# Kernel optimization log

Hardware: AMD Instinct MI355X
Metric: run time of the kernel (lower is better)

Reference implementation:

```python
import jax, jax.numpy as jnp
import numpy as np
from jax import lax

EPS = 1e-5  # torch BatchNorm2d default eps


def _binconv(x, w, b):
    # BinarizeConv2d: sign-binarize input and weight, dense conv, then add bias
    y = lax.conv_general_dilated(jnp.sign(x), jnp.sign(w), (2, 2), [(1, 1), (1, 1)],
                                 dimension_numbers=('NCHW', 'OIHW', 'NCHW'))
    return y + b[None, :, None, None]


def _bn(x, g, be):
    # BatchNorm2d in training mode: biased batch statistics over (N,H,W)
    m = jnp.mean(x, axis=(0, 2, 3), keepdims=True)
    v = jnp.mean((x - m) ** 2, axis=(0, 2, 3), keepdims=True)
    return (x - m) * (g[None, :, None, None] / jnp.sqrt(v + EPS)) + be[None, :, None, None]


def setup_inputs() -> dict:
    key = jax.random.key(0)
    ks = jax.random.split(key, 20)
    B = 8192
    d = {"x": jax.random.normal(ks[0], (B, 6, 32, 48), jnp.float32)}
    chans = [(12, 6), (24, 12), (48, 24), (96, 48)]
    i = 1
    for n, (co, ci) in enumerate(chans, 1):
        d[f"w{n}"] = jax.random.normal(ks[i], (co, ci, 5, 5), jnp.float32) * 0.1; i += 1
        d[f"b{n}"] = jax.random.normal(ks[i], (co,), jnp.float32) * 0.01; i += 1
        d[f"g{n}"] = jnp.ones((co,), jnp.float32)
        d[f"be{n}"] = jnp.zeros((co,), jnp.float32)
    d["wl"] = jax.random.normal(ks[i], (360, 192), jnp.float32) * 0.1; i += 1
    d["bl"] = jax.random.normal(ks[i], (360,), jnp.float32) * 0.01
    return d


def reference(x, w1, b1, g1, be1, w2, b2, g2, be2, w3, b3, g3, be3,
              w4, b4, g4, be4, wl, bl):
    x1 = jnp.clip(_bn(_binconv(x, w1, b1), g1, be1), 0.0, 1.0)
    x2 = jnp.clip(_bn(_binconv(x1, w2, b2), g2, be2), 0.0, 1.0)
    x3 = jnp.clip(_bn(_binconv(x2, w3, b3), g3, be3), 0.0, 1.0)
    x4 = jnp.clip(_bn(_binconv(x3, w4, b4), g4, be4), 0.0, 1.0)
    x4 = x4.reshape(-1, 192)  # (B, 96*1*2)
    # BinarizeLinear: in_features=192 != 784 so input is binarized too
    return jnp.sign(x4) @ jnp.sign(wl).T + bl
```

## Files before the change

### kernel.cpp

```cpp
#include <hip/hip_runtime.h>
#include <stdint.h>

typedef unsigned long long u64;
typedef uint32_t u32;
typedef uint16_t u16;

#define NIMG 8192

static const size_t O_TOT = 0;
static const size_t O_X1  = 4096;
static const size_t O_A2  = O_X1 + (size_t)NIMG*32*50*2;
static const size_t O_A3  = O_A2 + (size_t)NIMG*15*25*2;
static const size_t O_A4  = O_A3 + (size_t)NIMG*7*13*4;
static const size_t O_AL  = O_A4 + (size_t)NIMG*3*7*8;
static const size_t O_W1  = O_AL + (size_t)NIMG*3*8;
static const size_t O_W2  = O_W1 + 120*8;
static const size_t O_W3  = O_W2 + 240*8;
static const size_t O_W4  = O_W3 + 960*8;
static const size_t O_WL  = O_W4 + 3840*8;
static const size_t O_S   = O_WL + 2160*8;

__global__ void pack_w_k(const float* w1, const float* w2, const float* w3,
                         const float* w4, const float* wl,
                         u64* W1, u64* W2, u64* W3, u64* W4, u64* WL, u64* tot) {
  if (blockIdx.x == 5) {
    int t = threadIdx.x;
    tot[t] = 0; tot[t+256] = 0;
    return;
  }
  int u = blockIdx.x*256 + threadIdx.x;
  if (u < 60) {
    int co = u/5, kh = u%5;
    u64 wp=0, wn=0;
    for (int kw=0; kw<5; kw++) for (int ci=0; ci<6; ci++) {
      float v = w1[co*150 + ci*25 + kh*5 + kw];
      int pos = 6*kw + ci;
      if (v > 0.f) wp |= 1ull<<pos; else if (v < 0.f) wn |= 1ull<<pos;
    }
    W1[u*2]   = wp | (wn<<32);
    W1[u*2+1] = wn | (wp<<32);
  } else if (u < 180) {
    int t = u-60; int co=t/5, kh=t%5;
    u64 wp=0, wn=0;
    for (int kw=0; kw<5; kw++) for (int ci=0; ci<12; ci++) {
      float v = w2[co*300 + ci*25 + kh*5 + kw];
      int pos = 12*kw+ci;
      if (v>0.f) wp |= 1ull<<pos; else if (v<0.f) wn |= 1ull<<pos;
    }
    W2[t*2] = wp; W2[t*2+1] = wn;
  } else if (u < 420) {
    int t = u-180; int co=t/5, kh=t%5;
    u64 wp[2]={0,0}, wn[2]={0,0};
    for (int kw=0; kw<5; kw++) for (int ci=0; ci<24; ci++) {
      float v = w3[co*600 + ci*25 + kh*5 + kw];
      int pos = 24*kw+ci;
      if (v>0.f) wp[pos>>6] |= 1ull<<(pos&63); else if (v<0.f) wn[pos>>6] |= 1ull<<(pos&63);
    }
    W3[t*4]=wp[0]; W3[t*4+1]=wp[1]; W3[t*4+2]=wn[0]; W3[t*4+3]=wn[1];
  } else if (u < 900) {
    int t = u-420; int co=t/5, kh=t%5;
    u64 wp[4]={0,0,0,0}, wn[4]={0,0,0,0};
    for (int kw=0; kw<5; kw++) for (int ci=0; ci<48; ci++) {
      float v = w4[co*1200 + ci*25 + kh*5 + kw];
      int pos = 48*kw+ci;
      if (v>0.f) wp[pos>>6] |= 1ull<<(pos&63); else if (v<0.f) wn[pos>>6] |= 1ull<<(pos&63);
    }
    for (int j=0;j<4;j++){ W4[t*8+j]=wp[j]; W4[t*8+4+j]=wn[j]; }
  } else if (u < 1260) {
    int o = u-900;
    u64 wp[3]={0,0,0}, wn[3]={0,0,0};
    for (int k=0;k<192;k++){
      float v = wl[o*192+k];
      if (v>0.f) wp[k>>6] |= 1ull<<(k&63); else if (v<0.f) wn[k>>6] |= 1ull<<(k&63);
    }
    for (int j=0;j<3;j++){ WL[o*6+j]=wp[j]; WL[o*6+3+j]=wn[j]; }
  }
}

__global__ __launch_bounds__(256) void binx_k(const float* __restrict__ x, u16* __restrict__ X1) {
  int gid = blockIdx.x*256+threadIdx.x;
  int n = gid / 1536, r = gid % 1536, h = r/48, w = r%48;
  const float* xp = x + (size_t)n*9216 + h*48 + w;
  u32 v = 0;
  #pragma unroll
  for (int c=0;c<6;c++){ float t = xp[c*1536];
    v |= (t>0.f ? 1u:0u)<<c; v |= (t<0.f ? 1u:0u)<<(8+c); }
  u16* row = X1 + (size_t)n*1600 + h*50;
  row[w+1] = (u16)v;
  if (w==0)  row[0]  = 0;
  if (w==47) row[49] = 0;
}

__global__ __launch_bounds__(256) void conv1_k(const u16* __restrict__ X1, const u64* __restrict__ W1,
                                               u32* __restrict__ S1) {
  int pix = blockIdx.x*256+threadIdx.x;
  int n = pix/345, r = pix%345, oh = r/23, ow = r%23;
  int S[12];
  #pragma unroll
  for (int i=0;i<12;i++) S[i]=0;
  const u16* base = X1 + (size_t)n*1600;
  for (int kh=0; kh<5; kh++){
    int row = 2*oh-1+kh;
    if ((unsigned)row >= 32u) continue;
    const u16* p = base + row*50 + 2*ow;
    u64 xp=0, xn=0;
    #pragma unroll
    for (int i=0;i<5;i++){ u32 v = p[i];
      xp |= (u64)(v & 63u) << (6*i);
      xn |= (u64)(v >> 8)  << (6*i); }
    u64 X = xp | (xn<<32);
    const u64* wr = W1 + kh*2;
    #pragma unroll
    for (int co=0;co<12;co++)
      S[co] += __popcll(X & wr[co*10]) - __popcll(X & wr[co*10+1]);
  }
  u32* o = S1 + (size_t)pix*3;
  #pragma unroll
  for (int j=0;j<3;j++)
    o[j] = (u32)(S[4*j]&255) | ((u32)(S[4*j+1]&255)<<8) |
           ((u32)(S[4*j+2]&255)<<16) | ((u32)(S[4*j+3]&255)<<24);
}

__global__ __launch_bounds__(256) void conv2_k(const u16* __restrict__ A2, const u64* __restrict__ W2,
                                               short* __restrict__ S2) {
  int pix = blockIdx.x*256+threadIdx.x;
  int n = pix/77, r = pix%77, oh = r/11, ow = r%11;
  int S[24];
  #pragma unroll
  for (int i=0;i<24;i++) S[i]=0;
  const u16* base = A2 + (size_t)n*375;
  for (int kh=0; kh<5; kh++){
    int row = 2*oh-1+kh;
    if ((unsigned)row >= 15u) continue;
    const u16* p = base + row*25 + 2*ow;
    u64 X=0;
    #pragma unroll
    for (int i=0;i<5;i++) X |= (u64)p[i] << (12*i);
    const u64* wr = W2 + kh*2;
    #pragma unroll
    for (int co=0;co<24;co++)
      S[co] += __popcll(X & wr[co*10]) - __popcll(X & wr[co*10+1]);
  }
  short* o = S2 + (size_t)pix*24;
  #pragma unroll
  for (int co=0;co<24;co++) o[co] = (short)S[co];
}

__global__ __launch_bounds__(256) void conv3_k(const u32* __restrict__ A3, const u64* __restrict__ W3,
                                               short* __restrict__ S3) {
  int pix = blockIdx.x*256+threadIdx.x;
  int n = pix/15, r = pix%15, oh = r/5, ow = r%5;
  int S[48];
  #pragma unroll
  for (int i=0;i<48;i++) S[i]=0;
  const u32* base = A3 + (size_t)n*91;
  for (int kh=0; kh<5; kh++){
    int row = 2*oh-1+kh;
    if ((unsigned)row >= 7u) continue;
    const u32* p = base + row*13 + 2*ow;
    u64 a0=p[0],a1=p[1],a2=p[2],a3=p[3],a4=p[4];
    u64 x0 = a0 | (a1<<24) | (a2<<48);
    u64 x1 = (a2>>16) | (a3<<8) | (a4<<32);
    const u64* wr = W3 + kh*4;
    #pragma unroll
    for (int co=0;co<48;co++){
      const u64* q = wr + co*20;
      S[co] += __popcll(x0 & q[0]) + __popcll(x1 & q[1])
             - __popcll(x0 & q[2]) - __popcll(x1 & q[3]);
    }
  }
  short* o = S3 + (size_t)pix*48;
  #pragma unroll
  for (int co=0;co<48;co++) o[co] = (short)S[co];
}

__global__ __launch_bounds__(256) void conv4_k(const u64* __restrict__ A4, const u64* __restrict__ W4,
                                               short* __restrict__ S4) {
  int gid = blockIdx.x*256+threadIdx.x;
  int pix = gid>>2, grp = gid&3;
  int n = pix>>1, ow = pix&1;
  int S[24];
  #pragma unroll
  for (int i=0;i<24;i++) S[i]=0;
  const u64* base = A4 + (size_t)n*21;
  for (int kh=0; kh<5; kh++){
    int row = kh-1;
    if ((unsigned)row >= 3u) continue;
    const u64* p = base + row*7 + 2*ow;
    u64 a0=p[0],a1=p[1],a2=p[2],a3=p[3],a4=p[4];
    u64 x0 = a0 | (a1<<48);
    u64 x1 = (a1>>16) | (a2<<32);
    u64 x2 = (a2>>32) | (a3<<16);
    u64 x3 = a4;
    const u64* wr = W4 + kh*8;
    #pragma unroll
    for (int j=0;j<24;j++){
      const u64* q = wr + (grp*24+j)*40;
      S[j] += __popcll(x0&q[0]) + __popcll(x1&q[1]) + __popcll(x2&q[2]) + __popcll(x3&q[3])
            - __popcll(x0&q[4]) - __popcll(x1&q[5]) - __popcll(x2&q[6]) - __popcll(x3&q[7]);
    }
  }
  short* o = S4 + (size_t)pix*96 + grp*24;
  #pragma unroll
  for (int j=0;j<24;j++) o[j] = (short)S[j];
}

#define LSTR 265
template<int NR>
__device__ long long tree_reduce(const int (&vals)[NR], int* lds){
  int t = threadIdx.x;
  #pragma unroll
  for (int r=0;r<NR;r++) lds[r*LSTR + t] = vals[r];
  __syncthreads();
  if (t < NR*8) {
    int r = t % NR, seg = t / NR;
    const int* row = lds + r*LSTR + seg*32;
    int s = 0;
    #pragma unroll
    for (int i=0;i<32;i++) s += row[i];
    lds[r*LSTR + 256 + seg] = s;
  }
  __syncthreads();
  long long res = 0;
  if (t < NR) {
    const int* row = lds + t*LSTR + 256;
    int s = 0;
    #pragma unroll
    for (int i=0;i<8;i++) s += row[i];
    res = s;
  }
  __syncthreads();
  return res;
}

__global__ __launch_bounds__(256) void stats1_k(const u32* __restrict__ S1, u64* __restrict__ tot){
  __shared__ int lds[24*LSTR];
  int acc[12], q[12];
  #pragma unroll
  for (int i=0;i<12;i++){ acc[i]=0; q[i]=0; }
  int nt = gridDim.x*256;
  for (int p = blockIdx.x*256+threadIdx.x; p < NIMG*345; p += nt){
    u32 w0=S1[(size_t)p*3], w1=S1[(size_t)p*3+1], w2=S1[(size_t)p*3+2];
    #pragma unroll
    for (int c=0;c<12;c++){
      u32 w = (c<4)?w0:(c<8)?w1:w2;
      int v = (int)(w << ((3-(c&3))*8)) >> 24;
      acc[c]+=v; q[c]+=v*v;
    }
  }
  int vals[24];
  #pragma unroll
  for (int c=0;c<12;c++){ vals[c]=acc[c]; vals[12+c]=q[c]; }
  long long rs = tree_reduce<24>(vals, lds);
  int t = threadIdx.x;
  if (t < 12)       atomicAdd(&tot[t*2],        (u64)rs);
  else if (t < 24)  atomicAdd(&tot[(t-12)*2+1], (u64)rs);
}

__global__ __launch_bounds__(256) void stats2_k(const short* __restrict__ S, u64* __restrict__ tot){
  __shared__ int lds[24*LSTR];
  int acc[24], q[24];
  #pragma unroll
  for (int i=0;i<24;i++){ acc[i]=0; q[i]=0; }
  int nt = gridDim.x*256;
  for (int p = blockIdx.x*256+threadIdx.x; p < NIMG*77; p += nt){
    const int4* s4 = (const int4*)(S + (size_t)p*24);
    int4 A=s4[0], B=s4[1], Cc=s4[2];
    int w[12]={A.x,A.y,A.z,A.w,B.x,B.y,B.z,B.w,Cc.x,Cc.y,Cc.z,Cc.w};
    #pragma unroll
    for (int j=0;j<12;j++){
      int v0=(int)(short)(w[j]&0xffff), v1=w[j]>>16;
      acc[2*j]+=v0; q[2*j]+=v0*v0; acc[2*j+1]+=v1; q[2*j+1]+=v1*v1;
    }
  }
  long long rs = tree_reduce<24>(acc, lds);
  int t = threadIdx.x;
  if (t < 24) atomicAdd(&tot[t*2], (u64)rs);
  rs = tree_reduce<24>(q, lds);
  if (t < 24) atomicAdd(&tot[t*2+1], (u64)rs);
}

__global__ __launch_bounds__(256) void statsP_k(const short* __restrict__ S, u64* __restrict__ tot, int C){
  __shared__ int lds[24*LSTR];
  int pix = blockIdx.x*256+threadIdx.x;
  const short* s = S + (size_t)pix*C;
  int t = threadIdx.x;
  for (int c0=0; c0<C; c0+=24){
    const int4* s4 = (const int4*)(s + c0);
    int4 A=s4[0], B=s4[1], Cc=s4[2];
    int w[12]={A.x,A.y,A.z,A.w,B.x,B.y,B.z,B.w,Cc.x,Cc.y,Cc.z,Cc.w};
    int v[24];
    #pragma unroll
    for (int j=0;j<12;j++){ v[2*j]=(int)(short)(w[j]&0xffff); v[2*j+1]=w[j]>>16; }
    long long rs = tree_reduce<24>(v, lds);
    if (t < 24) atomicAdd(&tot[(c0+t)*2], (u64)rs);
    int vq[24];
    #pragma unroll
    for (int r=0;r<24;r++) vq[r]=v[r]*v[r];
    rs = tree_reduce<24>(vq, lds);
    if (t < 24) atomicAdd(&tot[(c0+t)*2+1], (u64)rs);
  }
}

template<int C>
__device__ void bn_params(const u64* tot, const float* g, const float* be, double cnt,
                          float* s_mu, float* s_k, float* s_be) {
  int t = threadIdx.x;
  if (t < C) {
    long long sum = (long long)tot[t*2];
    long long sq  = (long long)tot[t*2+1];
    double mu  = (double)sum / cnt;
    double var = (double)sq / cnt - mu*mu;
    double kk  = (double)g[t] / sqrt(var + 1e-5);
    s_mu[t] = (float)mu; s_k[t] = (float)kk; s_be[t] = be[t];
  }
  __syncthreads();
}

__global__ __launch_bounds__(256) void thresh1_k(const u32* __restrict__ S1, const u64* tot,
                                                 const float* g, const float* be, u16* __restrict__ A2){
  __shared__ float mu[12], kk[12], bb[12];
  bn_params<12>(tot, g, be, 2826240.0, mu, kk, bb);
  int pix = blockIdx.x*256+threadIdx.x;
  int n=pix/345, r=pix%345, oh=r/23, ow=r%23;
  const u32* s = S1 + (size_t)pix*3;
  u32 w0=s[0], w1=s[1], w2=s[2];
  u32 wv=0;
  #pragma unroll
  for (int c=0;c<12;c++){
    u32 w = (c<4) ? w0 : (c<8) ? w1 : w2;
    int sv = (int)(w << ((3-(c&3))*8)) >> 24;
    float v = ((float)sv-mu[c])*kk[c]+bb[c];
    wv |= (v>0.f?1u:0u)<<c;
  }
  u16* row = A2 + (size_t)n*375 + oh*25;
  row[ow+1] = (u16)wv;
  if (ow==0)  row[0]  = 0;
  if (ow==22) row[24] = 0;
}

__global__ __launch_bounds__(256) void thresh2_k(const short* __restrict__ S2, const u64* tot,
                                                 const float* g, const float* be, u32* __restrict__ A3){
  __shared__ float mu[24], kk[24], bb[24];
  bn_params<24>(tot, g, be, 630784.0, mu, kk, bb);
  int pix = blockIdx.x*256+threadIdx.x;
  int n=pix/77, r=pix%77, oh=r/11, ow=r%11;
  const short* s = S2 + (size_t)pix*24;
  u32 wv=0;
  #pragma unroll
  for (int c=0;c<24;c++){ float v = ((float)s[c]-mu[c])*kk[c]+bb[c]; wv |= (v>0.f?1u:0u)<<c; }
  u32* row = A3 + (size_t)n*91 + oh*13;
  row[ow+1] = wv;
  if (ow==0)  row[0]  = 0;
  if (ow==10) row[12] = 0;
}

__global__ __launch_bounds__(256) void thresh3_k(const short* __restrict__ S3, const u64* tot,
                                                 const float* g, const float* be, u64* __restrict__ A4){
  __shared__ float mu[48], kk[48], bb[48];
  bn_params<48>(tot, g, be, 122880.0, mu, kk, bb);
  int pix = blockIdx.x*256+threadIdx.x;
  int n=pix/15, r=pix%15, oh=r/5, ow=r%5;
  const short* s = S3 + (size_t)pix*48;
  u64 wv=0;
  #pragma unroll
  for (int c=0;c<48;c++){ float v = ((float)s[c]-mu[c])*kk[c]+bb[c]; wv |= (u64)(v>0.f?1u:0u)<<c; }
  u64* row = A4 + (size_t)n*21 + oh*7;
  row[ow+1] = wv;
  if (ow==0) row[0] = 0;
  if (ow==4) row[6] = 0;
}

__global__ __launch_bounds__(256) void thresh4_k(const short* __restrict__ S4, const u64* tot,
                                                 const float* g, const float* be, u64* __restrict__ aL){
  __shared__ float mu[96], kk[96], bb[96];
  bn_params<96>(tot, g, be, 16384.0, mu, kk, bb);
  int n = blockIdx.x*256+threadIdx.x;
  if (n >= NIMG) return;
  u64 a[3]={0,0,0};
  for (int w=0;w<2;w++){
    const short* s = S4 + ((size_t)n*2+w)*96;
    #pragma unroll
    for (int c=0;c<96;c++){
      float v = ((float)s[c]-mu[c])*kk[c]+bb[c];
      int k = c*2+w;
      if (v>0.f) a[k>>6] |= 1ull<<(k&63);
    }
  }
  aL[(size_t)n*3]=a[0]; aL[(size_t)n*3+1]=a[1]; aL[(size_t)n*3+2]=a[2];
}

__global__ __launch_bounds__(256) void linear_k(const u64* __restrict__ aL, const u64* __restrict__ WL,
                                                const float* __restrict__ bl, float* __restrict__ out){
  int gid = blockIdx.x*256+threadIdx.x;
  int o = gid%360, n = gid/360;
  const u64* a = aL + (size_t)n*3;
  const u64* w = WL + (size_t)o*6;
  int S = __popcll(a[0]&w[0]) + __popcll(a[1]&w[1]) + __popcll(a[2]&w[2])
        - __popcll(a[0]&w[3]) - __popcll(a[1]&w[4]) - __popcll(a[2]&w[5]);
  out[gid] = (float)S + bl[o];
}

extern "C" void kernel_launch(void* const* d_in, const int* in_sizes, int n_in,
                              void* d_out, int out_size, void* d_ws, size_t ws_size,
                              hipStream_t stream) {
  const float* x  = (const float*)d_in[0];
  const float* w1 = (const float*)d_in[1];
  const float* g1 = (const float*)d_in[3];
  const float* be1= (const float*)d_in[4];
  const float* w2 = (const float*)d_in[5];
  const float* g2 = (const float*)d_in[7];
  const float* be2= (const float*)d_in[8];
  const float* w3 = (const float*)d_in[9];
  const float* g3 = (const float*)d_in[11];
  const float* be3= (const float*)d_in[12];
  const float* w4 = (const float*)d_in[13];
  const float* g4 = (const float*)d_in[15];
  const float* be4= (const float*)d_in[16];
  const float* wl = (const float*)d_in[17];
  const float* bl = (const float*)d_in[18];

  char* ws = (char*)d_ws;
  u64* tot = (u64*)(ws + O_TOT);
  u16* X1  = (u16*)(ws + O_X1);
  u16* A2  = (u16*)(ws + O_A2);
  u32* A3  = (u32*)(ws + O_A3);
  u64* A4  = (u64*)(ws + O_A4);
  u64* aL  = (u64*)(ws + O_AL);
  u64* W1  = (u64*)(ws + O_W1);
  u64* W2  = (u64*)(ws + O_W2);
  u64* W3  = (u64*)(ws + O_W3);
  u64* W4  = (u64*)(ws + O_W4);
  u64* WL  = (u64*)(ws + O_WL);
  u32*   S1b = (u32*)(ws + O_S);
  short* Sb  = (short*)(ws + O_S);

  pack_w_k<<<6,256,0,stream>>>(w1,w2,w3,w4,wl, W1,W2,W3,W4,WL, tot);
  binx_k<<<49152,256,0,stream>>>(x, X1);

  conv1_k<<<11040,256,0,stream>>>(X1, W1, S1b);
  stats1_k<<<1024,256,0,stream>>>(S1b, tot+0);
  thresh1_k<<<11040,256,0,stream>>>(S1b, tot+0, g1, be1, A2);

  conv2_k<<<2464,256,0,stream>>>(A2, W2, Sb);
  stats2_k<<<512,256,0,stream>>>(Sb, tot+24);
  thresh2_k<<<2464,256,0,stream>>>(Sb, tot+24, g2, be2, A3);

  conv3_k<<<480,256,0,stream>>>(A3, W3, Sb);
  statsP_k<<<480,256,0,stream>>>(Sb, tot+72, 48);
  thresh3_k<<<480,256,0,stream>>>(Sb, tot+72, g3, be3, A4);

  conv4_k<<<256,256,0,stream>>>(A4, W4, Sb);
  statsP_k<<<64,256,0,stream>>>(Sb, tot+168, 96);
  thresh4_k<<<32,256,0,stream>>>(Sb, tot+168, g4, be4, aL);

  linear_k<<<11520,256,0,stream>>>(aL, WL, bl, (float*)d_out);
}
```

Baseline: 869.2 us.

## Fuse binarize, conv, BN stats and threshold into per-layer kernels

```diff
diff --git a/kernel.cpp b/kernel.cpp
--- a/kernel.cpp
+++ b/kernel.cpp
@@ -8,17 +8,13 @@
 #define NIMG 8192
 
 static const size_t O_TOT = 0;
-static const size_t O_X1  = 4096;
-static const size_t O_A2  = O_X1 + (size_t)NIMG*32*50*2;
-static const size_t O_A3  = O_A2 + (size_t)NIMG*15*25*2;
-static const size_t O_A4  = O_A3 + (size_t)NIMG*7*13*4;
-static const size_t O_AL  = O_A4 + (size_t)NIMG*3*7*8;
-static const size_t O_W1  = O_AL + (size_t)NIMG*3*8;
+static const size_t O_W1  = 4096;
 static const size_t O_W2  = O_W1 + 120*8;
 static const size_t O_W3  = O_W2 + 240*8;
 static const size_t O_W4  = O_W3 + 960*8;
 static const size_t O_WL  = O_W4 + 3840*8;
-static const size_t O_S   = O_WL + 2160*8;
+static const size_t O_SA  = 65536;
+static const size_t O_SB  = O_SA + (size_t)NIMG*345*12;
 
 __global__ void pack_w_k(const float* w1, const float* w2, const float* w3,
                          const float* w4, const float* wl,
@@ -77,234 +73,9 @@
   }
 }
 
-__global__ __launch_bounds__(256) void binx_k(const float* __restrict__ x, u16* __restrict__ X1) {
-  int gid = blockIdx.x*256+threadIdx.x;
-  int n = gid / 1536, r = gid % 1536, h = r/48, w = r%48;
-  const float* xp = x + (size_t)n*9216 + h*48 + w;
-  u32 v = 0;
-  #pragma unroll
-  for (int c=0;c<6;c++){ float t = xp[c*1536];
-    v |= (t>0.f ? 1u:0u)<<c; v |= (t<0.f ? 1u:0u)<<(8+c); }
-  u16* row = X1 + (size_t)n*1600 + h*50;
-  row[w+1] = (u16)v;
-  if (w==0)  row[0]  = 0;
-  if (w==47) row[49] = 0;
-}
-
-__global__ __launch_bounds__(256) void conv1_k(const u16* __restrict__ X1, const u64* __restrict__ W1,
-                                               u32* __restrict__ S1) {
-  int pix = blockIdx.x*256+threadIdx.x;
-  int n = pix/345, r = pix%345, oh = r/23, ow = r%23;
-  int S[12];
-  #pragma unroll
-  for (int i=0;i<12;i++) S[i]=0;
-  const u16* base = X1 + (size_t)n*1600;
-  for (int kh=0; kh<5; kh++){
-    int row = 2*oh-1+kh;
-    if ((unsigned)row >= 32u) continue;
-    const u16* p = base + row*50 + 2*ow;
-    u64 xp=0, xn=0;
-    #pragma unroll
-    for (int i=0;i<5;i++){ u32 v = p[i];
-      xp |= (u64)(v & 63u) << (6*i);
-      xn |= (u64)(v >> 8)  << (6*i); }
-    u64 X = xp | (xn<<32);
-    const u64* wr = W1 + kh*2;
-    #pragma unroll
-    for (int co=0;co<12;co++)
-      S[co] += __popcll(X & wr[co*10]) - __popcll(X & wr[co*10+1]);
-  }
-  u32* o = S1 + (size_t)pix*3;
-  #pragma unroll
-  for (int j=0;j<3;j++)
-    o[j] = (u32)(S[4*j]&255) | ((u32)(S[4*j+1]&255)<<8) |
-           ((u32)(S[4*j+2]&255)<<16) | ((u32)(S[4*j+3]&255)<<24);
-}
-
-__global__ __launch_bounds__(256) void conv2_k(const u16* __restrict__ A2, const u64* __restrict__ W2,
-                                               short* __restrict__ S2) {
-  int pix = blockIdx.x*256+threadIdx.x;
-  int n = pix/77, r = pix%77, oh = r/11, ow = r%11;
-  int S[24];
-  #pragma unroll
-  for (int i=0;i<24;i++) S[i]=0;
-  const u16* base = A2 + (size_t)n*375;
-  for (int kh=0; kh<5; kh++){
-    int row = 2*oh-1+kh;
-    if ((unsigned)row >= 15u) continue;
-    const u16* p = base + row*25 + 2*ow;
-    u64 X=0;
-    #pragma unroll
-    for (int i=0;i<5;i++) X |= (u64)p[i] << (12*i);
-    const u64* wr = W2 + kh*2;
-    #pragma unroll
-    for (int co=0;co<24;co++)
-      S[co] += __popcll(X & wr[co*10]) - __popcll(X & wr[co*10+1]);
-  }
-  short* o = S2 + (size_t)pix*24;
-  #pragma unroll
-  for (int co=0;co<24;co++) o[co] = (short)S[co];
-}
-
-__global__ __launch_bounds__(256) void conv3_k(const u32* __restrict__ A3, const u64* __restrict__ W3,
-                                               short* __restrict__ S3) {
-  int pix = blockIdx.x*256+threadIdx.x;
-  int n = pix/15, r = pix%15, oh = r/5, ow = r%5;
-  int S[48];
-  #pragma unroll
-  for (int i=0;i<48;i++) S[i]=0;
-  const u32* base = A3 + (size_t)n*91;
-  for (int kh=0; kh<5; kh++){
-    int row = 2*oh-1+kh;
-    if ((unsigned)row >= 7u) continue;
-    const u32* p = base + row*13 + 2*ow;
-    u64 a0=p[0],a1=p[1],a2=p[2],a3=p[3],a4=p[4];
-    u64 x0 = a0 | (a1<<24) | (a2<<48);
-    u64 x1 = (a2>>16) | (a3<<8) | (a4<<32);
-    const u64* wr = W3 + kh*4;
-    #pragma unroll
-    for (int co=0;co<48;co++){
-      const u64* q = wr + co*20;
-      S[co] += __popcll(x0 & q[0]) + __popcll(x1 & q[1])
-             - __popcll(x0 & q[2]) - __popcll(x1 & q[3]);
-    }
-  }
-  short* o = S3 + (size_t)pix*48;
-  #pragma unroll
-  for (int co=0;co<48;co++) o[co] = (short)S[co];
-}
-
-__global__ __launch_bounds__(256) void conv4_k(const u64* __restrict__ A4, const u64* __restrict__ W4,
-                                               short* __restrict__ S4) {
-  int gid = blockIdx.x*256+threadIdx.x;
-  int pix = gid>>2, grp = gid&3;
-  int n = pix>>1, ow = pix&1;
-  int S[24];
-  #pragma unroll
-  for (int i=0;i<24;i++) S[i]=0;
-  const u64* base = A4 + (size_t)n*21;
-  for (int kh=0; kh<5; kh++){
-    int row = kh-1;
-    if ((unsigned)row >= 3u) continue;
-    const u64* p = base + row*7 + 2*ow;
-    u64 a0=p[0],a1=p[1],a2=p[2],a3=p[3],a4=p[4];
-    u64 x0 = a0 | (a1<<48);
-    u64 x1 = (a1>>16) | (a2<<32);
-    u64 x2 = (a2>>32) | (a3<<16);
-    u64 x3 = a4;
-    const u64* wr = W4 + kh*8;
-    #pragma unroll
-    for (int j=0;j<24;j++){
-      const u64* q = wr + (grp*24+j)*40;
-      S[j] += __popcll(x0&q[0]) + __popcll(x1&q[1]) + __popcll(x2&q[2]) + __popcll(x3&q[3])
-            - __popcll(x0&q[4]) - __popcll(x1&q[5]) - __popcll(x2&q[6]) - __popcll(x3&q[7]);
-    }
-  }
-  short* o = S4 + (size_t)pix*96 + grp*24;
-  #pragma unroll
-  for (int j=0;j<24;j++) o[j] = (short)S[j];
-}
-
-#define LSTR 265
-template<int NR>
-__device__ long long tree_reduce(const int (&vals)[NR], int* lds){
-  int t = threadIdx.x;
-  #pragma unroll
-  for (int r=0;r<NR;r++) lds[r*LSTR + t] = vals[r];
-  __syncthreads();
-  if (t < NR*8) {
-    int r = t % NR, seg = t / NR;
-    const int* row = lds + r*LSTR + seg*32;
-    int s = 0;
-    #pragma unroll
-    for (int i=0;i<32;i++) s += row[i];
-    lds[r*LSTR + 256 + seg] = s;
-  }
-  __syncthreads();
-  long long res = 0;
-  if (t < NR) {
-    const int* row = lds + t*LSTR + 256;
-    int s = 0;
-    #pragma unroll
-    for (int i=0;i<8;i++) s += row[i];
-    res = s;
-  }
-  __syncthreads();
-  return res;
-}
-
-__global__ __launch_bounds__(256) void stats1_k(const u32* __restrict__ S1, u64* __restrict__ tot){
-  __shared__ int lds[24*LSTR];
-  int acc[12], q[12];
-  #pragma unroll
-  for (int i=0;i<12;i++){ acc[i]=0; q[i]=0; }
-  int nt = gridDim.x*256;
-  for (int p = blockIdx.x*256+threadIdx.x; p < NIMG*345; p += nt){
-    u32 w0=S1[(size_t)p*3], w1=S1[(size_t)p*3+1], w2=S1[(size_t)p*3+2];
-    #pragma unroll
-    for (int c=0;c<12;c++){
-      u32 w = (c<4)?w0:(c<8)?w1:w2;
-      int v = (int)(w << ((3-(c&3))*8)) >> 24;
-      acc[c]+=v; q[c]+=v*v;
-    }
-  }
-  int vals[24];
-  #pragma unroll
-  for (int c=0;c<12;c++){ vals[c]=acc[c]; vals[12+c]=q[c]; }
-  long long rs = tree_reduce<24>(vals, lds);
-  int t = threadIdx.x;
-  if (t < 12)       atomicAdd(&tot[t*2],        (u64)rs);
-  else if (t < 24)  atomicAdd(&tot[(t-12)*2+1], (u64)rs);
-}
-
-__global__ __launch_bounds__(256) void stats2_k(const short* __restrict__ S, u64* __restrict__ tot){
-  __shared__ int lds[24*LSTR];
-  int acc[24], q[24];
-  #pragma unroll
-  for (int i=0;i<24;i++){ acc[i]=0; q[i]=0; }
-  int nt = gridDim.x*256;
-  for (int p = blockIdx.x*256+threadIdx.x; p < NIMG*77; p += nt){
-    const int4* s4 = (const int4*)(S + (size_t)p*24);
-    int4 A=s4[0], B=s4[1], Cc=s4[2];
-    int w[12]={A.x,A.y,A.z,A.w,B.x,B.y,B.z,B.w,Cc.x,Cc.y,Cc.z,Cc.w};
-    #pragma unroll
-    for (int j=0;j<12;j++){
-      int v0=(int)(short)(w[j]&0xffff), v1=w[j]>>16;
-      acc[2*j]+=v0; q[2*j]+=v0*v0; acc[2*j+1]+=v1; q[2*j+1]+=v1*v1;
-    }
-  }
-  long long rs = tree_reduce<24>(acc, lds);
-  int t = threadIdx.x;
-  if (t < 24) atomicAdd(&tot[t*2], (u64)rs);
-  rs = tree_reduce<24>(q, lds);
-  if (t < 24) atomicAdd(&tot[t*2+1], (u64)rs);
-}
-
-__global__ __launch_bounds__(256) void statsP_k(const short* __restrict__ S, u64* __restrict__ tot, int C){
-  __shared__ int lds[24*LSTR];
-  int pix = blockIdx.x*256+threadIdx.x;
-  const short* s = S + (size_t)pix*C;
-  int t = threadIdx.x;
-  for (int c0=0; c0<C; c0+=24){
-    const int4* s4 = (const int4*)(s + c0);
-    int4 A=s4[0], B=s4[1], Cc=s4[2];
-    int w[12]={A.x,A.y,A.z,A.w,B.x,B.y,B.z,B.w,Cc.x,Cc.y,Cc.z,Cc.w};
-    int v[24];
-    #pragma unroll
-    for (int j=0;j<12;j++){ v[2*j]=(int)(short)(w[j]&0xffff); v[2*j+1]=w[j]>>16; }
-    long long rs = tree_reduce<24>(v, lds);
-    if (t < 24) atomicAdd(&tot[(c0+t)*2], (u64)rs);
-    int vq[24];
-    #pragma unroll
-    for (int r=0;r<24;r++) vq[r]=v[r]*v[r];
-    rs = tree_reduce<24>(vq, lds);
-    if (t < 24) atomicAdd(&tot[(c0+t)*2+1], (u64)rs);
-  }
-}
-
 template<int C>
-__device__ void bn_params(const u64* tot, const float* g, const float* be, double cnt,
-                          float* s_mu, float* s_k, float* s_be) {
+__device__ inline void bn_params(const u64* tot, const float* g, const float* be, double cnt,
+                                 float* s_mu, float* s_k, float* s_be) {
   int t = threadIdx.x;
   if (t < C) {
     long long sum = (long long)tot[t*2];
@@ -317,88 +88,304 @@
   __syncthreads();
 }
 
-__global__ __launch_bounds__(256) void thresh1_k(const u32* __restrict__ S1, const u64* tot,
-                                                 const float* g, const float* be, u16* __restrict__ A2){
+template<int NV, int LANES, int C>
+__device__ inline void block_stats(int (&v)[NV], u64* tot, int* rl) {
+  #pragma unroll
+  for (int o = 32; o >= LANES; o >>= 1)
+    #pragma unroll
+    for (int r = 0; r < NV; r++) v[r] += __shfl_down(v[r], o, 64);
+  int lane = threadIdx.x & 63, wid = threadIdx.x >> 6;
+  if (lane < LANES) {
+    #pragma unroll
+    for (int r = 0; r < NV; r++) rl[(lane*NV + r)*4 + wid] = v[r];
+  }
+  __syncthreads();
+  int t = threadIdx.x;
+  if (t < LANES*NV) {
+    int g = t / NV, r = t % NV;
+    int s = rl[t*4] + rl[t*4+1] + rl[t*4+2] + rl[t*4+3];
+    int cc = g*C + (r < C ? r : r - C);
+    atomicAdd(&tot[cc*2 + (r < C ? 0 : 1)], (u64)(long long)s);
+  }
+}
+
+__global__ __launch_bounds__(256) void layer1_k(const float* __restrict__ x,
+    const u64* __restrict__ W1, u32* __restrict__ S1, u64* __restrict__ tot) {
+  __shared__ u16 X1[2][32][50];
+  __shared__ int rl[24*4];
+  int t = threadIdx.x;
+  int acc[12], sq[12];
+  #pragma unroll
+  for (int i=0;i<12;i++){ acc[i]=0; sq[i]=0; }
+  for (int pr=0; pr<2; pr++) {
+    int n0 = blockIdx.x*4 + pr*2;
+    for (int u=t; u<3072; u+=256) {
+      int img = (u >= 1536) ? 1 : 0;
+      int q = u - img*1536;
+      int h = q/48, w = q%48;
+      const float* xb = x + (size_t)(n0+img)*9216 + q;
+      u32 v = 0;
+      #pragma unroll
+      for (int c=0;c<6;c++){ float f = xb[c*1536];
+        v |= (f>0.f ? 1u:0u)<<c; v |= (f<0.f ? 1u:0u)<<(8+c); }
+      X1[img][h][w+1] = (u16)v;
+      if (w==0)  X1[img][h][0]  = 0;
+      if (w==47) X1[img][h][49] = 0;
+    }
+    __syncthreads();
+    for (int u=t; u<690; u+=256) {
+      int img = (u >= 345) ? 1 : 0;
+      int p = u - img*345;
+      int oh = p/23, ow = p%23;
+      int P[12], T = 0;
+      #pragma unroll
+      for (int i=0;i<12;i++) P[i]=0;
+      for (int kh=0; kh<5; kh++) {
+        int row = 2*oh-1+kh;
+        if ((unsigned)row >= 32u) continue;
+        const u16* xr = &X1[img][row][2*ow];
+        u64 xp=0, xn=0;
+        #pragma unroll
+        for (int i=0;i<5;i++){ u32 v = xr[i];
+          xp |= (u64)(v & 63u) << (6*i);
+          xn |= (u64)(v >> 8)  << (6*i); }
+        u64 X = xp | (xn<<32);
+        T += __popcll(X);
+        const u64* wr = W1 + kh*2;
+        #pragma unroll
+        for (int co=0;co<12;co++)
+          P[co] += __popcll(X & wr[co*10]);
+      }
+      int S[12];
+      #pragma unroll
+      for (int co=0;co<12;co++){ S[co] = 2*P[co] - T; acc[co]+=S[co]; sq[co]+=S[co]*S[co]; }
+      u32* o = S1 + ((size_t)(n0+img)*345 + p)*3;
+      #pragma unroll
+      for (int j=0;j<3;j++)
+        o[j] = (u32)(S[4*j]&255) | ((u32)(S[4*j+1]&255)<<8) |
+               ((u32)(S[4*j+2]&255)<<16) | ((u32)(S[4*j+3]&255)<<24);
+    }
+    __syncthreads();
+  }
+  int v[24];
+  #pragma unroll
+  for (int c=0;c<12;c++){ v[c]=acc[c]; v[12+c]=sq[c]; }
+  block_stats<24,1,12>(v, tot, rl);
+}
+
+__global__ __launch_bounds__(256) void layer2_k(const u32* __restrict__ S1, u64* tot,
+    const float* __restrict__ g, const float* __restrict__ be,
+    const u64* __restrict__ W2, short* __restrict__ S2) {
   __shared__ float mu[12], kk[12], bb[12];
   bn_params<12>(tot, g, be, 2826240.0, mu, kk, bb);
-  int pix = blockIdx.x*256+threadIdx.x;
-  int n=pix/345, r=pix%345, oh=r/23, ow=r%23;
-  const u32* s = S1 + (size_t)pix*3;
-  u32 w0=s[0], w1=s[1], w2=s[2];
-  u32 wv=0;
-  #pragma unroll
-  for (int c=0;c<12;c++){
-    u32 w = (c<4) ? w0 : (c<8) ? w1 : w2;
-    int sv = (int)(w << ((3-(c&3))*8)) >> 24;
-    float v = ((float)sv-mu[c])*kk[c]+bb[c];
-    wv |= (v>0.f?1u:0u)<<c;
-  }
-  u16* row = A2 + (size_t)n*375 + oh*25;
-  row[ow+1] = (u16)wv;
-  if (ow==0)  row[0]  = 0;
-  if (ow==22) row[24] = 0;
-}
-
-__global__ __launch_bounds__(256) void thresh2_k(const short* __restrict__ S2, const u64* tot,
-                                                 const float* g, const float* be, u32* __restrict__ A3){
+  __shared__ u16 A2[8][15][25];
+  __shared__ int rl[48*4];
+  int t = threadIdx.x;
+  int n0 = blockIdx.x*8;
+  for (int u=t; u<8*345; u+=256) {
+    int img = u/345, p = u%345;
+    int oh = p/23, ow = p%23;
+    const u32* s = S1 + ((size_t)(n0+img)*345 + p)*3;
+    u32 w0=s[0], w1=s[1], w2v=s[2];
+    u32 wv = 0;
+    #pragma unroll
+    for (int c=0;c<12;c++){
+      u32 w = (c<4) ? w0 : (c<8) ? w1 : w2v;
+      int sv = (int)(w << ((3-(c&3))*8)) >> 24;
+      float v = ((float)sv-mu[c])*kk[c]+bb[c];
+      wv |= (v>0.f?1u:0u)<<c;
+    }
+    A2[img][oh][ow+1] = (u16)wv;
+    if (ow==0)  A2[img][oh][0]  = 0;
+    if (ow==22) A2[img][oh][24] = 0;
+  }
+  __syncthreads();
+  int acc[24], sq[24];
+  #pragma unroll
+  for (int i=0;i<24;i++){ acc[i]=0; sq[i]=0; }
+  for (int u=t; u<8*77; u+=256) {
+    int img = u/77, p = u%77;
+    int oh = p/11, ow = p%11;
+    int P[24], T = 0;
+    #pragma unroll
+    for (int i=0;i<24;i++) P[i]=0;
+    for (int kh=0; kh<5; kh++) {
+      int row = 2*oh-1+kh;
+      if ((unsigned)row >= 15u) continue;
+      const u16* xr = &A2[img][row][2*ow];
+      u64 X = 0;
+      #pragma unroll
+      for (int i=0;i<5;i++) X |= (u64)xr[i] << (12*i);
+      T += __popcll(X);
+      const u64* wr = W2 + kh*2;
+      #pragma unroll
+      for (int co=0;co<24;co++)
+        P[co] += __popcll(X & wr[co*10]);
+    }
+    short* o = S2 + ((size_t)(n0+img)*77 + p)*24;
+    #pragma unroll
+    for (int co=0;co<24;co++){ int sv = 2*P[co]-T; o[co]=(short)sv; acc[co]+=sv; sq[co]+=sv*sv; }
+  }
+  int v[48];
+  #pragma unroll
+  for (int c=0;c<24;c++){ v[c]=acc[c]; v[24+c]=sq[c]; }
+  block_stats<48,1,24>(v, tot+24, rl);
+}
+
+__global__ __launch_bounds__(256) void layer3_k(const short* __restrict__ S2, u64* tot,
+    const float* __restrict__ g, const float* __restrict__ be,
+    const u64* __restrict__ W3, short* __restrict__ S3) {
   __shared__ float mu[24], kk[24], bb[24];
-  bn_params<24>(tot, g, be, 630784.0, mu, kk, bb);
-  int pix = blockIdx.x*256+threadIdx.x;
-  int n=pix/77, r=pix%77, oh=r/11, ow=r%11;
-  const short* s = S2 + (size_t)pix*24;
-  u32 wv=0;
-  #pragma unroll
-  for (int c=0;c<24;c++){ float v = ((float)s[c]-mu[c])*kk[c]+bb[c]; wv |= (v>0.f?1u:0u)<<c; }
-  u32* row = A3 + (size_t)n*91 + oh*13;
-  row[ow+1] = wv;
-  if (ow==0)  row[0]  = 0;
-  if (ow==10) row[12] = 0;
-}
-
-__global__ __launch_bounds__(256) void thresh3_k(const short* __restrict__ S3, const u64* tot,
-                                                 const float* g, const float* be, u64* __restrict__ A4){
+  bn_params<24>(tot+24, g, be, 630784.0, mu, kk, bb);
+  __shared__ u32 A3[16][7][13];
+  __shared__ int rl[2*48*4];
+  int t = threadIdx.x;
+  int n0 = blockIdx.x*16;
+  for (int u=t; u<16*77; u+=256) {
+    int img = u/77, p = u%77;
+    int oh = p/11, ow = p%11;
+    const int4* s4 = (const int4*)(S2 + ((size_t)(n0+img)*77 + p)*24);
+    int4 A=s4[0], B=s4[1], Cv=s4[2];
+    int wvals[12]={A.x,A.y,A.z,A.w,B.x,B.y,B.z,B.w,Cv.x,Cv.y,Cv.z,Cv.w};
+    u32 wv = 0;
+    #pragma unroll
+    for (int j=0;j<12;j++){
+      int v0=(int)(short)(wvals[j]&0xffff), v1=wvals[j]>>16;
+      float f0 = ((float)v0-mu[2*j])*kk[2*j]+bb[2*j];
+      float f1 = ((float)v1-mu[2*j+1])*kk[2*j+1]+bb[2*j+1];
+      wv |= (f0>0.f?1u:0u)<<(2*j);
+      wv |= (f1>0.f?1u:0u)<<(2*j+1);
+    }
+    A3[img][oh][ow+1] = wv;
+    if (ow==0)  A3[img][oh][0]  = 0;
+    if (ow==10) A3[img][oh][12] = 0;
+  }
+  __syncthreads();
+  int acc[24], sq[24];
+  #pragma unroll
+  for (int i=0;i<24;i++){ acc[i]=0; sq[i]=0; }
+  int grp = t & 1;
+  for (int u=t; u<16*30; u+=256) {
+    int img = u/30, rem = u%30;
+    int px = rem>>1;
+    int oh = px/5, ow = px%5;
+    int P[24], T = 0;
+    #pragma unroll
+    for (int i=0;i<24;i++) P[i]=0;
+    for (int kh=0; kh<5; kh++) {
+      int row = 2*oh-1+kh;
+      if ((unsigned)row >= 7u) continue;
+      const u32* pr = &A3[img][row][2*ow];
+      u64 a0=pr[0],a1=pr[1],a2=pr[2],a3=pr[3],a4=pr[4];
+      u64 x0 = a0 | (a1<<24) | (a2<<48);
+      u64 x1 = (a2>>16) | (a3<<8) | (a4<<32);
+      T += __popcll(x0) + __popcll(x1);
+      const u64* wr = W3 + kh*4;
+      #pragma unroll
+      for (int j=0;j<24;j++){
+        const u64* qq = wr + (grp*24+j)*20;
+        P[j] += __popcll(x0&qq[0]) + __popcll(x1&qq[1]);
+      }
+    }
+    short* o = S3 + ((size_t)(n0+img)*15 + px)*48 + grp*24;
+    #pragma unroll
+    for (int j=0;j<24;j++){ int sv = 2*P[j]-T; o[j]=(short)sv; acc[j]+=sv; sq[j]+=sv*sv; }
+  }
+  int v[48];
+  #pragma unroll
+  for (int c=0;c<24;c++){ v[c]=acc[c]; v[24+c]=sq[c]; }
+  block_stats<48,2,24>(v, tot+72, rl);
+}
+
+__global__ __launch_bounds__(256) void layer4_k(const short* __restrict__ S3, u64* tot,
+    const float* __restrict__ g, const float* __restrict__ be,
+    const u64* __restrict__ W4, short* __restrict__ S4) {
   __shared__ float mu[48], kk[48], bb[48];
-  bn_params<48>(tot, g, be, 122880.0, mu, kk, bb);
-  int pix = blockIdx.x*256+threadIdx.x;
-  int n=pix/15, r=pix%15, oh=r/5, ow=r%5;
-  const short* s = S3 + (size_t)pix*48;
-  u64 wv=0;
-  #pragma unroll
-  for (int c=0;c<48;c++){ float v = ((float)s[c]-mu[c])*kk[c]+bb[c]; wv |= (u64)(v>0.f?1u:0u)<<c; }
-  u64* row = A4 + (size_t)n*21 + oh*7;
-  row[ow+1] = wv;
-  if (ow==0) row[0] = 0;
-  if (ow==4) row[6] = 0;
-}
-
-__global__ __launch_bounds__(256) void thresh4_k(const short* __restrict__ S4, const u64* tot,
-                                                 const float* g, const float* be, u64* __restrict__ aL){
+  bn_params<48>(tot+72, g, be, 122880.0, mu, kk, bb);
+  __shared__ u64 A4[32][3][7];
+  __shared__ int rl[4*48*4];
+  int t = threadIdx.x;
+  int n0 = blockIdx.x*32;
+  for (int u=t; u<32*15; u+=256) {
+    int img = u/15, px = u%15;
+    int oh = px/5, ow = px%5;
+    const int4* s4 = (const int4*)(S3 + ((size_t)(n0+img)*15 + px)*48);
+    u64 wv = 0;
+    #pragma unroll
+    for (int q4=0;q4<6;q4++){
+      int4 w4v = s4[q4];
+      int wa[4]={w4v.x,w4v.y,w4v.z,w4v.w};
+      #pragma unroll
+      for (int j=0;j<4;j++){
+        int c = q4*8 + j*2;
+        int v0=(int)(short)(wa[j]&0xffff), v1=wa[j]>>16;
+        float f0=((float)v0-mu[c])*kk[c]+bb[c];
+        float f1=((float)v1-mu[c+1])*kk[c+1]+bb[c+1];
+        wv |= (u64)(f0>0.f?1u:0u)<<c;
+        wv |= (u64)(f1>0.f?1u:0u)<<(c+1);
+      }
+    }
+    A4[img][oh][ow+1] = wv;
+    if (ow==0) A4[img][oh][0] = 0;
+    if (ow==4) A4[img][oh][6] = 0;
+  }
+  __syncthreads();
+  int img = t>>3, unit = t&7, ow = unit>>2, grp = unit&3;
+  int P[24], T = 0;
+  #pragma unroll
+  for (int i=0;i<24;i++) P[i]=0;
+  for (int kh=0; kh<5; kh++) {
+    int row = kh-1;
+    if ((unsigned)row >= 3u) continue;
+    const u64* pr = &A4[img][row][2*ow];
+    u64 a0=pr[0],a1=pr[1],a2=pr[2],a3=pr[3],a4=pr[4];
+    u64 x0 = a0 | (a1<<48);
+    u64 x1 = (a1>>16) | (a2<<32);
+    u64 x2 = (a2>>32) | (a3<<16);
+    u64 x3 = a4;
+    T += __popcll(x0)+__popcll(x1)+__popcll(x2)+__popcll(x3);
+    const u64* wr = W4 + kh*8;
+    #pragma unroll
+    for (int j=0;j<24;j++){
+      const u64* qq = wr + (grp*24+j)*40;
+      P[j] += __popcll(x0&qq[0])+__popcll(x1&qq[1])+__popcll(x2&qq[2])+__popcll(x3&qq[3]);
+    }
+  }
+  short* o = S4 + ((size_t)(n0+img)*2 + ow)*96 + grp*24;
+  int v[48];
+  #pragma unroll
+  for (int j=0;j<24;j++){ int sv = 2*P[j]-T; o[j]=(short)sv; v[j]=sv; v[24+j]=sv*sv; }
+  block_stats<48,4,24>(v, tot+168, rl);
+}
+
+__global__ __launch_bounds__(256) void layer5_k(const short* __restrict__ S4, u64* tot,
+    const float* __restrict__ g, const float* __restrict__ be,
+    const u64* __restrict__ WL, const float* __restrict__ bl, float* __restrict__ out) {
   __shared__ float mu[96], kk[96], bb[96];
-  bn_params<96>(tot, g, be, 16384.0, mu, kk, bb);
-  int n = blockIdx.x*256+threadIdx.x;
-  if (n >= NIMG) return;
-  u64 a[3]={0,0,0};
-  for (int w=0;w<2;w++){
-    const short* s = S4 + ((size_t)n*2+w)*96;
-    #pragma unroll
-    for (int c=0;c<96;c++){
-      float v = ((float)s[c]-mu[c])*kk[c]+bb[c];
-      int k = c*2+w;
-      if (v>0.f) a[k>>6] |= 1ull<<(k&63);
-    }
-  }
-  aL[(size_t)n*3]=a[0]; aL[(size_t)n*3+1]=a[1]; aL[(size_t)n*3+2]=a[2];
-}
-
-__global__ __launch_bounds__(256) void linear_k(const u64* __restrict__ aL, const u64* __restrict__ WL,
-                                                const float* __restrict__ bl, float* __restrict__ out){
-  int gid = blockIdx.x*256+threadIdx.x;
-  int o = gid%360, n = gid/360;
-  const u64* a = aL + (size_t)n*3;
-  const u64* w = WL + (size_t)o*6;
-  int S = __popcll(a[0]&w[0]) + __popcll(a[1]&w[1]) + __popcll(a[2]&w[2])
-        - __popcll(a[0]&w[3]) - __popcll(a[1]&w[4]) - __popcll(a[2]&w[5]);
-  out[gid] = (float)S + bl[o];
+  bn_params<96>(tot+168, g, be, 16384.0, mu, kk, bb);
+  __shared__ u64 AL[4][3];
+  __shared__ int ALT[4];
+  int t = threadIdx.x, lane = t & 63, wid = t >> 6;
+  int n0 = blockIdx.x*4;
+  for (int ch = wid; ch < 12; ch += 4) {
+    int img = ch/3, word = ch%3;
+    int k = word*64 + lane;
+    int c = k>>1, wp = k&1;
+    int sv = S4[((size_t)(n0+img)*2 + wp)*96 + c];
+    float f = ((float)sv-mu[c])*kk[c]+bb[c];
+    u64 m = __ballot(f > 0.f);
+    if (lane == 0) AL[img][word] = m;
+  }
+  __syncthreads();
+  if (t < 4) ALT[t] = __popcll(AL[t][0]) + __popcll(AL[t][1]) + __popcll(AL[t][2]);
+  __syncthreads();
+  for (int u=t; u<4*360; u+=256) {
+    int img = u/360, o = u%360;
+    const u64* w = WL + (size_t)o*6;
+    u64 a0=AL[img][0], a1=AL[img][1], a2=AL[img][2];
+    int S = 2*(__popcll(a0&w[0]) + __popcll(a1&w[1]) + __popcll(a2&w[2])) - ALT[img];
+    out[(size_t)(n0+img)*360 + o] = (float)S + bl[o];
+  }
 }
 
 extern "C" void kernel_launch(void* const* d_in, const int* in_sizes, int n_in,
@@ -422,37 +409,20 @@
 
   char* ws = (char*)d_ws;
   u64* tot = (u64*)(ws + O_TOT);
-  u16* X1  = (u16*)(ws + O_X1);
-  u16* A2  = (u16*)(ws + O_A2);
-  u32* A3  = (u32*)(ws + O_A3);
-  u64* A4  = (u64*)(ws + O_A4);
-  u64* aL  = (u64*)(ws + O_AL);
   u64* W1  = (u64*)(ws + O_W1);
   u64* W2  = (u64*)(ws + O_W2);
   u64* W3  = (u64*)(ws + O_W3);
   u64* W4  = (u64*)(ws + O_W4);
   u64* WL  = (u64*)(ws + O_WL);
-  u32*   S1b = (u32*)(ws + O_S);
-  short* Sb  = (short*)(ws + O_S);
+  u32*   S1 = (u32*)(ws + O_SA);
+  short* S2 = (short*)(ws + O_SB);
+  short* S3 = (short*)(ws + O_SA);
+  short* S4 = (short*)(ws + O_SB);
 
   pack_w_k<<<6,256,0,stream>>>(w1,w2,w3,w4,wl, W1,W2,W3,W4,WL, tot);
-  binx_k<<<49152,256,0,stream>>>(x, X1);
-
-  conv1_k<<<11040,256,0,stream>>>(X1, W1, S1b);
-  stats1_k<<<1024,256,0,stream>>>(S1b, tot+0);
-  thresh1_k<<<11040,256,0,stream>>>(S1b, tot+0, g1, be1, A2);
-
-  conv2_k<<<2464,256,0,stream>>>(A2, W2, Sb);
-  stats2_k<<<512,256,0,stream>>>(Sb, tot+24);
-  thresh2_k<<<2464,256,0,stream>>>(Sb, tot+24, g2, be2, A3);
-
-  conv3_k<<<480,256,0,stream>>>(A3, W3, Sb);
-  statsP_k<<<480,256,0,stream>>>(Sb, tot+72, 48);
-  thresh3_k<<<480,256,0,stream>>>(Sb, tot+72, g3, be3, A4);
-
-  conv4_k<<<256,256,0,stream>>>(A4, W4, Sb);
-  statsP_k<<<64,256,0,stream>>>(Sb, tot+168, 96);
-  thresh4_k<<<32,256,0,stream>>>(Sb, tot+168, g4, be4, aL);
-
-  linear_k<<<11520,256,0,stream>>>(aL, WL, bl, (float*)d_out);
-}
+  layer1_k<<<2048,256,0,stream>>>(x, W1, S1, tot);
+  layer2_k<<<1024,256,0,stream>>>(S1, tot, g1, be1, W2, S2);
+  layer3_k<<<512,256,0,stream>>>(S2, tot, g2, be2, W3, S3);
+  layer4_k<<<256,256,0,stream>>>(S3, tot, g3, be3, W4, S4);
+  layer5_k<<<2048,256,0,stream>>>(S4, tot, g4, be4, WL, bl, (float*)d_out);
+}
```

After: 732.6 us. -15.7%, faster.
